# Performance work log

Hardware: AMD Instinct MI355X
Metric: run time of the kernel (lower is better)

## Reference

```python
import jax, jax.numpy as jnp
import numpy as np

N_HEAD = 16
D_IN = 1024
D_OUT = 1024
B, T = 2, 2048
HEAD_DIM = D_OUT // N_HEAD


def setup_inputs() -> dict:
    key = jax.random.key(0)
    ks = jax.random.split(key, 8)
    Q = jax.random.normal(ks[0], (B, T, D_IN), dtype=jnp.float32)
    K = jax.random.normal(ks[1], (B, T, D_IN), dtype=jnp.float32)
    V = jax.random.normal(ks[2], (B, T, D_IN), dtype=jnp.float32)
    mask = jax.random.randint(ks[3], (B, T, T), 0, 2, dtype=jnp.int32)
    s_in = 1.0 / np.sqrt(D_IN)
    s_out = 1.0 / np.sqrt(D_OUT)
    Wq = jax.random.uniform(ks[4], (D_IN, D_OUT), jnp.float32, -s_in, s_in)
    Wk = jax.random.uniform(ks[5], (D_IN, D_OUT), jnp.float32, -s_in, s_in)
    Wv = jax.random.uniform(ks[6], (D_IN, D_OUT), jnp.float32, -s_in, s_in)
    Wo = jax.random.uniform(ks[7], (D_OUT, D_OUT), jnp.float32, -s_out, s_out)
    return {"Q": Q, "K": K, "V": V, "mask": mask,
            "Wq": Wq, "Wk": Wk, "Wv": Wv, "Wo": Wo}


def _split_heads(x):
    b, t, _ = x.shape
    return x.reshape(b, t, N_HEAD, HEAD_DIM).transpose(0, 2, 1, 3)  # [B,H,T,hd]


def reference(Q, K, V, mask, Wq, Wk, Wv, Wo):
    q = _split_heads(Q @ Wq)
    k = _split_heads(K @ Wk)
    v = _split_heads(V @ Wv)
    scale = 1.0 / jnp.sqrt(jnp.float32(HEAD_DIM))  # Q.size(-1) after head split
    scores = jnp.einsum('bhqd,bhkd->bhqk', q, k) * scale  # [B,H,T,T]
    m = mask[:, None, :, :]  # expand over heads
    scores = jnp.where(m == 0, jnp.float32(-1e9), scores)
    attn = jax.nn.softmax(scores, axis=-1)
    z = jnp.einsum('bhqk,bhkd->bhqd', attn, v)  # [B,H,T,hd]
    z = z.transpose(0, 2, 1, 3).reshape(Q.shape[0], T, D_OUT)
    return z @ Wo
```

## Files before the change

### kernel.cpp

```cpp
#include <hip/hip_runtime.h>
#include <math.h>

#define DIN 1024
#define DOUT 1024
#define NHEAD 16
#define HDIM 64
#define BATCH 2
#define TSEQ 2048
#define MROWS (BATCH * TSEQ)

typedef unsigned short u16;
typedef __attribute__((ext_vector_type(8))) short short8;
typedef __attribute__((ext_vector_type(4))) float f32x4;
typedef __attribute__((ext_vector_type(4))) unsigned short us4;

__device__ __forceinline__ void f32_to_bf16pair(float x, u16& hi, u16& lo) {
  unsigned u = __float_as_uint(x);
  unsigned r = (u + 0x7fffu + ((u >> 16) & 1u)) & 0xffff0000u;
  hi = (u16)(r >> 16);
  float rem = x - __uint_as_float(r);
  unsigned u2 = __float_as_uint(rem);
  lo = (u16)((u2 + 0x7fffu + ((u2 >> 16) & 1u)) >> 16);
}

__device__ __forceinline__ void gld_lds16(const void* g, void* l) {
  __builtin_amdgcn_global_load_lds(
      (__attribute__((address_space(1))) void*)g,
      (__attribute__((address_space(3))) void*)l, 16, 0, 0);
}

__global__ __launch_bounds__(256) void splitA(
    const float* __restrict__ S0, const float* __restrict__ S1,
    const float* __restrict__ S2, u16* __restrict__ H0, u16* __restrict__ L0,
    u16* __restrict__ H1, u16* __restrict__ L1, u16* __restrict__ H2,
    u16* __restrict__ L2) {
  const int z = blockIdx.y;
  const float* S = z == 0 ? S0 : z == 1 ? S1 : S2;
  u16* H = z == 0 ? H0 : z == 1 ? H1 : H2;
  u16* L = z == 0 ? L0 : z == 1 ? L1 : L2;
  const size_t i = ((size_t)blockIdx.x * 256 + threadIdx.x) * 4;
  float4 v = *(const float4*)&S[i];
  us4 h4, l4;
  u16 hh, ll;
  f32_to_bf16pair(v.x, hh, ll);
  h4[0] = hh; l4[0] = ll;
  f32_to_bf16pair(v.y, hh, ll);
  h4[1] = hh; l4[1] = ll;
  f32_to_bf16pair(v.z, hh, ll);
  h4[2] = hh; l4[2] = ll;
  f32_to_bf16pair(v.w, hh, ll);
  h4[3] = hh; l4[3] = ll;
  *(us4*)&H[i] = h4;
  *(us4*)&L[i] = l4;
}

__global__ __launch_bounds__(256) void splitWt(
    const float* __restrict__ W0, const float* __restrict__ W1,
    const float* __restrict__ W2, const float* __restrict__ W3,
    u16* __restrict__ H0, u16* __restrict__ L0, u16* __restrict__ H1,
    u16* __restrict__ L1, u16* __restrict__ H2, u16* __restrict__ L2,
    u16* __restrict__ H3, u16* __restrict__ L3) {
  const int z = blockIdx.z;
  const float* W = z == 0 ? W0 : z == 1 ? W1 : z == 2 ? W2 : W3;
  u16* H = z == 0 ? H0 : z == 1 ? H1 : z == 2 ? H2 : H3;
  u16* L = z == 0 ? L0 : z == 1 ? L1 : z == 2 ? L2 : L3;
  __shared__ float ts[64][68];
  const int tid = threadIdx.x;
  const int k0 = blockIdx.y * 64, n0 = blockIdx.x * 64;
  {
    const int kl = tid >> 2, nc = (tid & 3) * 16;
#pragma unroll
    for (int c = 0; c < 4; ++c)
      *(float4*)&ts[kl][nc + c * 4] =
          *(const float4*)&W[(size_t)(k0 + kl) * DOUT + n0 + nc + c * 4];
  }
  __syncthreads();
  const int nl = tid >> 2, kc = (tid & 3) * 16;
#pragma unroll
  for (int g = 0; g < 4; ++g) {
    us4 h4, l4;
#pragma unroll
    for (int j = 0; j < 4; ++j) {
      u16 hh, ll;
      f32_to_bf16pair(ts[kc + g * 4 + j][nl], hh, ll);
      h4[j] = hh;
      l4[j] = ll;
    }
    const size_t idx = (size_t)(n0 + nl) * DIN + k0 + kc + g * 4;
    *(us4*)&H[idx] = h4;
    *(us4*)&L[idx] = l4;
  }
}

struct GemmPtrs {
  const u16* Ah;
  const u16* Al;
  const u16* Bh;
  const u16* Bl;
  u16* Oh;
  u16* Ol;
  int mode;
};
struct GemmArgs {
  GemmPtrs p[3];
};

__global__ __launch_bounds__(256) void gemm_qkv(GemmArgs args) {
  const GemmPtrs P = args.p[blockIdx.z];
  __shared__ alignas(16) u16 Abuf[128 * 64];
  __shared__ alignas(16) u16 Bbuf[128 * 64];
  const int tid = threadIdx.x;
  const int w = tid >> 6, lane = tid & 63;
  const int lr = lane & 15, qd = lane >> 4;
  const int mw = w >> 1, nw = w & 1;
  const int n0 = blockIdx.x * 128, m0 = blockIdx.y * 128;

  const u16* gA[4];
  const u16* gB[4];
  u16* lA[4];
  u16* lB[4];
  {
    const int cl = lane & 7;
#pragma unroll
    for (int is = 0; is < 4; ++is) {
      const int row = is * 32 + w * 8 + (lane >> 3);
      const int cg = cl ^ (row & 7);
      gA[is] = (cg < 4 ? P.Ah : P.Al) + (size_t)(m0 + row) * DIN + (cg & 3) * 8;
      gB[is] = (cg < 4 ? P.Bh : P.Bl) + (size_t)(n0 + row) * DIN + (cg & 3) * 8;
      lA[is] = Abuf + (size_t)(is * 32 + w * 8) * 64;
      lB[is] = Bbuf + (size_t)(is * 32 + w * 8) * 64;
    }
  }

  f32x4 acc[4][4] = {};

  for (int kt = 0; kt < 32; ++kt) {
    __syncthreads();
#pragma unroll
    for (int is = 0; is < 4; ++is) {
      gld_lds16(gA[is], lA[is]);
      gld_lds16(gB[is], lB[is]);
      gA[is] += 32;
      gB[is] += 32;
    }
    __syncthreads();

    short8 af[4][2], bf[4][2];
#pragma unroll
    for (int t = 0; t < 4; ++t) {
      const int ra = mw * 64 + t * 16 + lr;
      af[t][0] = *(const short8*)&Abuf[ra * 64 + ((qd ^ (ra & 7)) << 3)];
      af[t][1] = *(const short8*)&Abuf[ra * 64 + (((qd + 4) ^ (ra & 7)) << 3)];
      const int rb = nw * 64 + t * 16 + lr;
      bf[t][0] = *(const short8*)&Bbuf[rb * 64 + ((qd ^ (rb & 7)) << 3)];
      bf[t][1] = *(const short8*)&Bbuf[rb * 64 + (((qd + 4) ^ (rb & 7)) << 3)];
    }
#pragma unroll
    for (int mt = 0; mt < 4; ++mt)
#pragma unroll
      for (int nt = 0; nt < 4; ++nt) {
        acc[mt][nt] = __builtin_amdgcn_mfma_f32_16x16x32_bf16(
            af[mt][0], bf[nt][0], acc[mt][nt], 0, 0, 0);
        acc[mt][nt] = __builtin_amdgcn_mfma_f32_16x16x32_bf16(
            af[mt][0], bf[nt][1], acc[mt][nt], 0, 0, 0);
        acc[mt][nt] = __builtin_amdgcn_mfma_f32_16x16x32_bf16(
            af[mt][1], bf[nt][0], acc[mt][nt], 0, 0, 0);
      }
  }

#pragma unroll
  for (int mt = 0; mt < 4; ++mt)
#pragma unroll
    for (int nt = 0; nt < 4; ++nt)
#pragma unroll
      for (int r = 0; r < 4; ++r) {
        const float val = acc[mt][nt][r];
        const int gm = m0 + mw * 64 + mt * 16 + qd * 4 + r;
        const int gn = n0 + nw * 64 + nt * 16 + lr;
        u16 hh16, ll16;
        f32_to_bf16pair(val, hh16, ll16);
        const int bb = gm >> 11, t = gm & 2047;
        const int h = gn >> 6, d = gn & 63;
        size_t idx;
        if (P.mode == 0)
          idx = (((size_t)(bb * NHEAD + h) * TSEQ) + t) * HDIM + d;
        else
          idx = (((size_t)(bb * NHEAD + h) * HDIM) + d) * TSEQ + t;
        P.Oh[idx] = hh16;
        P.Ol[idx] = ll16;
      }
}

__global__ __launch_bounds__(256) void gemm_out(
    const u16* __restrict__ Ah, const u16* __restrict__ Al,
    const u16* __restrict__ Bh, const u16* __restrict__ Bl,
    float* __restrict__ C0, float* __restrict__ C1) {
  float* Of = blockIdx.z == 0 ? C0 : C1;
  const int koff = blockIdx.z * 512;
  __shared__ alignas(16) u16 Abuf[128 * 64];
  __shared__ alignas(16) u16 Bbuf[128 * 64];
  const int tid = threadIdx.x;
  const int w = tid >> 6, lane = tid & 63;
  const int lr = lane & 15, qd = lane >> 4;
  const int mw = w >> 1, nw = w & 1;
  const int n0 = blockIdx.x * 128, m0 = blockIdx.y * 128;

  const u16* gA[4];
  const u16* gB[4];
  u16* lA[4];
  u16* lB[4];
  {
    const int cl = lane & 7;
#pragma unroll
    for (int is = 0; is < 4; ++is) {
      const int row = is * 32 + w * 8 + (lane >> 3);
      const int cg = cl ^ (row & 7);
      gA[is] = (cg < 4 ? Ah : Al) + (size_t)(m0 + row) * DIN + (cg & 3) * 8 + koff;
      gB[is] = (cg < 4 ? Bh : Bl) + (size_t)(n0 + row) * DIN + (cg & 3) * 8 + koff;
      lA[is] = Abuf + (size_t)(is * 32 + w * 8) * 64;
      lB[is] = Bbuf + (size_t)(is * 32 + w * 8) * 64;
    }
  }

  f32x4 acc[4][4] = {};

  for (int kt = 0; kt < 16; ++kt) {
    __syncthreads();
#pragma unroll
    for (int is = 0; is < 4; ++is) {
      gld_lds16(gA[is], lA[is]);
      gld_lds16(gB[is], lB[is]);
      gA[is] += 32;
      gB[is] += 32;
    }
    __syncthreads();

    short8 af[4][2], bf[4][2];
#pragma unroll
    for (int t = 0; t < 4; ++t) {
      const int ra = mw * 64 + t * 16 + lr;
      af[t][0] = *(const short8*)&Abuf[ra * 64 + ((qd ^ (ra & 7)) << 3)];
      af[t][1] = *(const short8*)&Abuf[ra * 64 + (((qd + 4) ^ (ra & 7)) << 3)];
      const int rb = nw * 64 + t * 16 + lr;
      bf[t][0] = *(const short8*)&Bbuf[rb * 64 + ((qd ^ (rb & 7)) << 3)];
      bf[t][1] = *(const short8*)&Bbuf[rb * 64 + (((qd + 4) ^ (rb & 7)) << 3)];
    }
#pragma unroll
    for (int mt = 0; mt < 4; ++mt)
#pragma unroll
      for (int nt = 0; nt < 4; ++nt) {
        acc[mt][nt] = __builtin_amdgcn_mfma_f32_16x16x32_bf16(
            af[mt][0], bf[nt][0], acc[mt][nt], 0, 0, 0);
        acc[mt][nt] = __builtin_amdgcn_mfma_f32_16x16x32_bf16(
            af[mt][0], bf[nt][1], acc[mt][nt], 0, 0, 0);
        acc[mt][nt] = __builtin_amdgcn_mfma_f32_16x16x32_bf16(
            af[mt][1], bf[nt][0], acc[mt][nt], 0, 0, 0);
      }
  }

#pragma unroll
  for (int mt = 0; mt < 4; ++mt)
#pragma unroll
    for (int nt = 0; nt < 4; ++nt)
#pragma unroll
      for (int r = 0; r < 4; ++r) {
        const int gm = m0 + mw * 64 + mt * 16 + qd * 4 + r;
        const int gn = n0 + nw * 64 + nt * 16 + lr;
        Of[(size_t)gm * DOUT + gn] = acc[mt][nt][r];
      }
}

__global__ __launch_bounds__(256) void sumC(const float* __restrict__ A,
                                            const float* __restrict__ B,
                                            float* __restrict__ O) {
  const size_t i = ((size_t)blockIdx.x * 256 + threadIdx.x) * 4;
  float4 a = *(const float4*)&A[i];
  float4 b = *(const float4*)&B[i];
  *(float4*)&O[i] = make_float4(a.x + b.x, a.y + b.y, a.z + b.z, a.w + b.w);
}

template <int MODE>
__global__ __launch_bounds__(256) void gemm64(const float* __restrict__ A,
                                              const float* __restrict__ W,
                                              void* __restrict__ Y0,
                                              void* __restrict__ Y1) {
  __shared__ float As[16][68];
  __shared__ float Bs[16][68];
  const int tid = threadIdx.x;
  const int tx = tid & 15, ty = tid >> 4;
  const int r0 = ty * 4, c0 = tx * 4;
  const int gm0 = blockIdx.x * 64;
  const int gn0 = blockIdx.y * 64;
  const int am = tid >> 2;
  const int ak0 = (tid & 3) * 4;
  const int bk = tid >> 4;
  const int bc = (tid & 15) * 4;
  float acc[4][4] = {};
  for (int k0 = 0; k0 < DIN; k0 += 16) {
    __syncthreads();
    alignas(16) float av[4];
    *(float4*)av = *(const float4*)&A[(size_t)(gm0 + am) * DIN + k0 + ak0];
    As[ak0 + 0][am] = av[0];
    As[ak0 + 1][am] = av[1];
    As[ak0 + 2][am] = av[2];
    As[ak0 + 3][am] = av[3];
    *(float4*)&Bs[bk][bc] = *(const float4*)&W[(size_t)(k0 + bk) * DOUT + gn0 + bc];
    __syncthreads();
#pragma unroll
    for (int kk = 0; kk < 16; ++kk) {
      alignas(16) float a[4], b[4];
      *(float4*)a = *(const float4*)&As[kk][r0];
      *(float4*)b = *(const float4*)&Bs[kk][c0];
#pragma unroll
      for (int i = 0; i < 4; ++i)
#pragma unroll
        for (int j = 0; j < 4; ++j) acc[i][j] += a[i] * b[j];
    }
  }
  if constexpr (MODE == 1) {
    float* Y = (float*)Y0;
#pragma unroll
    for (int i = 0; i < 4; ++i) {
      float4 o = make_float4(acc[i][0], acc[i][1], acc[i][2], acc[i][3]);
      *(float4*)&Y[(size_t)(gm0 + r0 + i) * DOUT + gn0 + c0] = o;
    }
  } else if constexpr (MODE == 0) {
    u16* Yh = (u16*)Y0;
    u16* Yl = (u16*)Y1;
    const int bb = gm0 >> 11, tb = gm0 & 2047, h = gn0 >> 6;
#pragma unroll
    for (int i = 0; i < 4; ++i) {
      us4 h4, l4;
#pragma unroll
      for (int j = 0; j < 4; ++j) {
        u16 hh, ll;
        f32_to_bf16pair(acc[i][j], hh, ll);
        h4[j] = hh;
        l4[j] = ll;
      }
      size_t idx = (((size_t)(bb * NHEAD + h) * TSEQ) + tb + r0 + i) * HDIM + c0;
      *(us4*)&Yh[idx] = h4;
      *(us4*)&Yl[idx] = l4;
    }
  } else {
    __shared__ float ts[64][68];
#pragma unroll
    for (int i = 0; i < 4; ++i) {
      float4 o = make_float4(acc[i][0], acc[i][1], acc[i][2], acc[i][3]);
      *(float4*)&ts[r0 + i][c0] = o;
    }
    __syncthreads();
    u16* Yh = (u16*)Y0;
    u16* Yl = (u16*)Y1;
    const int bb = gm0 >> 11, tb = gm0 & 2047, h = gn0 >> 6;
    const int d = tid >> 2;
    const int t0 = (tid & 3) * 16;
#pragma unroll
    for (int g = 0; g < 4; ++g) {
      us4 h4, l4;
#pragma unroll
      for (int j = 0; j < 4; ++j) {
        u16 hh, ll;
        f32_to_bf16pair(ts[t0 + g * 4 + j][d], hh, ll);
        h4[j] = hh;
        l4[j] = ll;
      }
      size_t idx = (((size_t)(bb * NHEAD + h) * HDIM) + d) * TSEQ + tb + t0 + g * 4;
      *(us4*)&Yh[idx] = h4;
      *(us4*)&Yl[idx] = l4;
    }
  }
}

template <int EPI>
__global__ __launch_bounds__(256, 4) void attn64q(
    const u16* __restrict__ qh, const u16* __restrict__ ql,
    const u16* __restrict__ kh, const u16* __restrict__ kl,
    const u16* __restrict__ vh, const u16* __restrict__ vl,
    const int* __restrict__ mask, float* __restrict__ zf,
    u16* __restrict__ zh, u16* __restrict__ zl) {
  __shared__ alignas(16) u16 lds_k[2][64 * 64];
  __shared__ alignas(16) u16 lds_v[2][64 * 64];
  __shared__ alignas(16) u16 lds_p[4][16 * 64];
  const int tid = threadIdx.x;
  const int w = tid >> 6, lane = tid & 63;
  const int lr = lane & 15, qd = lane >> 4;
  const int L = blockIdx.x;
  const int bh = (L & 7) + 8 * ((L >> 3) & 3);
  const int qt0 = (L >> 5) * 64;
  const int bb = bh >> 4, hh = bh & 15;
  const int wq0 = qt0 + w * 16;
  const size_t bh_off = (size_t)bh * TSEQ * HDIM;

  short8 qf[2][2];
#pragma unroll
  for (int ks = 0; ks < 2; ++ks) {
    const size_t off = bh_off + (size_t)(wq0 + lr) * HDIM + ks * 32 + qd * 8;
    qf[ks][0] = *(const short8*)(qh + off);
    qf[ks][1] = *(const short8*)(ql + off);
  }

  f32x4 zacc[4] = {};
  float lsum[4] = {};

  const u16* ssrc = (w == 0 ? kh : w == 1 ? kl : w == 2 ? vh : vl) + bh_off;
  u16* sdst = (w < 2) ? &lds_k[w][0] : &lds_v[w - 2][0];
  const bool isk = (w < 2);
  const int srow = lane >> 3, scl = lane & 7;
  const int* mrow = mask + ((size_t)bb * TSEQ + wq0 + qd * 4) * TSEQ + lr;

  for (int kt0 = 0; kt0 < TSEQ; kt0 += 64) {
    __syncthreads();
#pragma unroll
    for (int is = 0; is < 8; ++is) {
      const int row = is * 8 + srow;
      const int cg = scl ^ (row & 7);
      const u16* src = isk ? ssrc + (size_t)(kt0 + row) * HDIM + cg * 8
                           : ssrc + (size_t)row * TSEQ + kt0 + cg * 8;
      gld_lds16(src, sdst + is * 512);
    }
    __syncthreads();

    int mv[4][4];
#pragma unroll
    for (int r = 0; r < 4; ++r) {
      const int* mr = mrow + (size_t)r * TSEQ + kt0;
#pragma unroll
      for (int nt = 0; nt < 4; ++nt) mv[nt][r] = mr[nt * 16];
    }

    f32x4 sacc[4] = {};
#pragma unroll
    for (int ks = 0; ks < 2; ++ks)
#pragma unroll
      for (int nt = 0; nt < 4; ++nt) {
        const int krow = nt * 16 + lr;
        const int chunk = (((ks * 4 + qd) ^ (krow & 7)) << 3);
        short8 bhf = *(const short8*)&lds_k[0][krow * 64 + chunk];
        short8 blf = *(const short8*)&lds_k[1][krow * 64 + chunk];
        sacc[nt] = __builtin_amdgcn_mfma_f32_16x16x32_bf16(qf[ks][0], bhf,
                                                           sacc[nt], 0, 0, 0);
        sacc[nt] = __builtin_amdgcn_mfma_f32_16x16x32_bf16(qf[ks][0], blf,
                                                           sacc[nt], 0, 0, 0);
        sacc[nt] = __builtin_amdgcn_mfma_f32_16x16x32_bf16(qf[ks][1], bhf,
                                                           sacc[nt], 0, 0, 0);
      }

    u16* pw = &lds_p[w][0];
#pragma unroll
    for (int nt = 0; nt < 4; ++nt)
#pragma unroll
      for (int r = 0; r < 4; ++r) {
        float s = sacc[nt][r];
        s = mv[nt][r] ? s * 0.125f : -1.0e9f;
        float p = __expf(s);
        unsigned u = (__float_as_uint(p) + 0x8000u) & 0xffff0000u;
        lsum[r] += __uint_as_float(u);
        const int prow = qd * 4 + r;
        const int pcol = nt * 16 + lr;
        pw[prow * 64 + ((((pcol >> 3) ^ (prow & 7)) << 3)) + (pcol & 7)] =
            (u16)(u >> 16);
      }

#pragma unroll
    for (int ks = 0; ks < 2; ++ks) {
      const int chunkp = (((ks * 4 + qd) ^ (lr & 7)) << 3);
      short8 pf = *(const short8*)&pw[lr * 64 + chunkp];
#pragma unroll
      for (int nt = 0; nt < 4; ++nt) {
        const int vrow = nt * 16 + lr;
        const int chunk = (((ks * 4 + qd) ^ (vrow & 7)) << 3);
        short8 vhf = *(const short8*)&lds_v[0][vrow * 64 + chunk];
        short8 vlf = *(const short8*)&lds_v[1][vrow * 64 + chunk];
        zacc[nt] = __builtin_amdgcn_mfma_f32_16x16x32_bf16(pf, vhf, zacc[nt],
                                                           0, 0, 0);
        zacc[nt] = __builtin_amdgcn_mfma_f32_16x16x32_bf16(pf, vlf, zacc[nt],
                                                           0, 0, 0);
      }
    }
  }

#pragma unroll
  for (int r = 0; r < 4; ++r) {
    float v = lsum[r];
#pragma unroll
    for (int off = 1; off < 16; off <<= 1) v += __shfl_xor(v, off);
    lsum[r] = 1.0f / v;
  }
#pragma unroll
  for (int r = 0; r < 4; ++r) {
    const int qrow = wq0 + qd * 4 + r;
#pragma unroll
    for (int nt = 0; nt < 4; ++nt) {
      const float val = zacc[nt][r] * lsum[r];
      const size_t idx =
          ((size_t)bb * TSEQ + qrow) * DOUT + hh * HDIM + nt * 16 + lr;
      if (EPI == 0) {
        zf[idx] = val;
      } else {
        u16 hh16, ll16;
        f32_to_bf16pair(val, hh16, ll16);
        zh[idx] = hh16;
        zl[idx] = ll16;
      }
    }
  }
}

extern "C" void kernel_launch(void* const* d_in, const int* in_sizes, int n_in,
                              void* d_out, int out_size, void* d_ws,
                              size_t ws_size, hipStream_t stream) {
  const float* Q = (const float*)d_in[0];
  const float* K = (const float*)d_in[1];
  const float* V = (const float*)d_in[2];
  const int* mask = (const int*)d_in[3];
  const float* Wq = (const float*)d_in[4];
  const float* Wk = (const float*)d_in[5];
  const float* Wv = (const float*)d_in[6];
  const float* Wo = (const float*)d_in[7];
  float* out = (float*)d_out;
  dim3 blk(256);

  if (ws_size >= (size_t)134217728) {
    u16* base = (u16*)d_ws;
    auto U = [&](size_t mib) { return base + mib * 524288; };
    u16 *Qh = U(0), *Ql = U(8), *Kh = U(16), *Kl = U(24), *Vh = U(32),
        *Vl = U(40);
    u16 *Wqh = U(48), *Wql = U(50), *Wkh = U(52), *Wkl = U(54), *Wvh = U(56),
        *Wvl = U(58), *Woh = U(60), *Wol = U(62);
    u16 *qh = U(64), *ql = U(72), *kh = U(80), *kl = U(88), *vth = U(96),
        *vtl = U(104);
    u16 *zh = U(112), *zl = U(120);
    float* C0 = (float*)U(0);
    float* C1 = (float*)U(16);

    splitA<<<dim3(4096, 3), blk, 0, stream>>>(Q, K, V, Qh, Ql, Kh, Kl, Vh, Vl);
    splitWt<<<dim3(16, 16, 4), blk, 0, stream>>>(Wq, Wk, Wv, Wo, Wqh, Wql, Wkh,
                                                 Wkl, Wvh, Wvl, Woh, Wol);
    GemmArgs ga;
    ga.p[0] = {Qh, Ql, Wqh, Wql, qh, ql, 0};
    ga.p[1] = {Kh, Kl, Wkh, Wkl, kh, kl, 0};
    ga.p[2] = {Vh, Vl, Wvh, Wvl, vth, vtl, 2};
    gemm_qkv<<<dim3(8, 32, 3), blk, 0, stream>>>(ga);
    attn64q<1><<<dim3(1024), blk, 0, stream>>>(qh, ql, kh, kl, vth, vtl, mask,
                                               nullptr, zh, zl);
    gemm_out<<<dim3(8, 32, 2), blk, 0, stream>>>(zh, zl, Woh, Wol, C0, C1);
    sumC<<<dim3(4096), blk, 0, stream>>>(C0, C1, out);
  } else {
    const size_t NE = (size_t)MROWS * DOUT;
    u16* qhb = (u16*)d_ws;
    u16* qlb = qhb + NE;
    u16* khb = qlb + NE;
    u16* klb = khb + NE;
    u16* vth = klb + NE;
    u16* vtl = vth + NE;
    float* zb = (float*)(vtl + NE);
    dim3 gg(MROWS / 64, DOUT / 64);
    gemm64<0><<<gg, blk, 0, stream>>>(Q, Wq, qhb, qlb);
    gemm64<0><<<gg, blk, 0, stream>>>(K, Wk, khb, klb);
    gemm64<2><<<gg, blk, 0, stream>>>(V, Wv, vth, vtl);
    attn64q<0><<<dim3(1024), blk, 0, stream>>>(qhb, qlb, khb, klb, vth, vtl,
                                               mask, zb, nullptr, nullptr);
    gemm64<1><<<gg, blk, 0, stream>>>(zb, Wo, (void*)out, nullptr);
  }
}
```

Measured before the change: 409.6 us.

## Fuse fp32 input bf16 split into QKV GEMM and bit-pack attention mask

The QKV GEMM now loads fp32 activations straight into LDS and splits them into bf16 hi/lo pairs in registers, so the separate splitA pass and its writes and re-reads of hi/lo arrays go away. A new mask_pack kernel packs the int32 mask into 64-bit ballot words, so the attention kernel reads 1 bit per mask entry instead of 4 bytes. The small-workspace fallback path is removed. The trade-off is redundant conversion ALU work in every GEMM tile (each A tile is re-split by every N-block) plus one extra launch for mask packing.

```diff
diff --git a/kernel.cpp b/kernel.cpp
--- a/kernel.cpp
+++ b/kernel.cpp
@@ -10,6 +10,7 @@
 #define MROWS (BATCH * TSEQ)
 
 typedef unsigned short u16;
+typedef unsigned long long u64;
 typedef __attribute__((ext_vector_type(8))) short short8;
 typedef __attribute__((ext_vector_type(4))) float f32x4;
 typedef __attribute__((ext_vector_type(4))) unsigned short us4;
@@ -29,29 +30,18 @@
       (__attribute__((address_space(3))) void*)l, 16, 0, 0);
 }
 
-__global__ __launch_bounds__(256) void splitA(
-    const float* __restrict__ S0, const float* __restrict__ S1,
-    const float* __restrict__ S2, u16* __restrict__ H0, u16* __restrict__ L0,
-    u16* __restrict__ H1, u16* __restrict__ L1, u16* __restrict__ H2,
-    u16* __restrict__ L2) {
-  const int z = blockIdx.y;
-  const float* S = z == 0 ? S0 : z == 1 ? S1 : S2;
-  u16* H = z == 0 ? H0 : z == 1 ? H1 : H2;
-  u16* L = z == 0 ? L0 : z == 1 ? L1 : L2;
-  const size_t i = ((size_t)blockIdx.x * 256 + threadIdx.x) * 4;
-  float4 v = *(const float4*)&S[i];
-  us4 h4, l4;
-  u16 hh, ll;
-  f32_to_bf16pair(v.x, hh, ll);
-  h4[0] = hh; l4[0] = ll;
-  f32_to_bf16pair(v.y, hh, ll);
-  h4[1] = hh; l4[1] = ll;
-  f32_to_bf16pair(v.z, hh, ll);
-  h4[2] = hh; l4[2] = ll;
-  f32_to_bf16pair(v.w, hh, ll);
-  h4[3] = hh; l4[3] = ll;
-  *(us4*)&H[i] = h4;
-  *(us4*)&L[i] = l4;
+__global__ __launch_bounds__(256) void mask_pack(const int* __restrict__ mask,
+                                                 u64* __restrict__ bits) {
+  const int gw = blockIdx.x * 4 + (threadIdx.x >> 6);
+  const int lane = threadIdx.x & 63;
+  const int* row = mask + (size_t)gw * TSEQ;
+  u64* orow = bits + (size_t)gw * (TSEQ / 64);
+#pragma unroll 4
+  for (int kt = 0; kt < TSEQ / 64; ++kt) {
+    int m = row[kt * 64 + lane];
+    u64 b = __ballot(m != 0);
+    if (lane == 0) orow[kt] = b;
+  }
 }
 
 __global__ __launch_bounds__(256) void splitWt(
@@ -92,22 +82,21 @@
   }
 }
 
-struct GemmPtrs {
-  const u16* Ah;
-  const u16* Al;
+struct QkvPtrs {
+  const float* Af;
   const u16* Bh;
   const u16* Bl;
   u16* Oh;
   u16* Ol;
   int mode;
 };
-struct GemmArgs {
-  GemmPtrs p[3];
+struct QkvArgs {
+  QkvPtrs p[3];
 };
 
-__global__ __launch_bounds__(256) void gemm_qkv(GemmArgs args) {
-  const GemmPtrs P = args.p[blockIdx.z];
-  __shared__ alignas(16) u16 Abuf[128 * 64];
+__global__ __launch_bounds__(256) void gemm_qkv(QkvArgs args) {
+  const QkvPtrs P = args.p[blockIdx.z];
+  __shared__ alignas(16) float Abuf[128 * 32];
   __shared__ alignas(16) u16 Bbuf[128 * 64];
   const int tid = threadIdx.x;
   const int w = tid >> 6, lane = tid & 63;
@@ -115,9 +104,9 @@
   const int mw = w >> 1, nw = w & 1;
   const int n0 = blockIdx.x * 128, m0 = blockIdx.y * 128;
 
-  const u16* gA[4];
+  const float* gA[4];
   const u16* gB[4];
-  u16* lA[4];
+  float* lA[4];
   u16* lB[4];
   {
     const int cl = lane & 7;
@@ -125,9 +114,9 @@
     for (int is = 0; is < 4; ++is) {
       const int row = is * 32 + w * 8 + (lane >> 3);
       const int cg = cl ^ (row & 7);
-      gA[is] = (cg < 4 ? P.Ah : P.Al) + (size_t)(m0 + row) * DIN + (cg & 3) * 8;
+      gA[is] = P.Af + (size_t)(m0 + row) * DIN + cg * 4;
       gB[is] = (cg < 4 ? P.Bh : P.Bl) + (size_t)(n0 + row) * DIN + (cg & 3) * 8;
-      lA[is] = Abuf + (size_t)(is * 32 + w * 8) * 64;
+      lA[is] = Abuf + (size_t)(is * 32 + w * 8) * 32;
       lB[is] = Bbuf + (size_t)(is * 32 + w * 8) * 64;
     }
   }
@@ -145,26 +134,41 @@
     }
     __syncthreads();
 
-    short8 af[4][2], bf[4][2];
+    short8 afh[4], afl[4];
 #pragma unroll
     for (int t = 0; t < 4; ++t) {
       const int ra = mw * 64 + t * 16 + lr;
-      af[t][0] = *(const short8*)&Abuf[ra * 64 + ((qd ^ (ra & 7)) << 3)];
-      af[t][1] = *(const short8*)&Abuf[ra * 64 + (((qd + 4) ^ (ra & 7)) << 3)];
+      const float* rp = &Abuf[ra * 32];
+      f32x4 a0 = *(const f32x4*)&rp[(((2 * qd) ^ (ra & 7)) * 4)];
+      f32x4 a1 = *(const f32x4*)&rp[(((2 * qd + 1) ^ (ra & 7)) * 4)];
+#pragma unroll
+      for (int j = 0; j < 4; ++j) {
+        u16 hh, ll;
+        f32_to_bf16pair(a0[j], hh, ll);
+        afh[t][j] = (short)hh;
+        afl[t][j] = (short)ll;
+        f32_to_bf16pair(a1[j], hh, ll);
+        afh[t][4 + j] = (short)hh;
+        afl[t][4 + j] = (short)ll;
+      }
+    }
+    short8 bfh[4], bfl[4];
+#pragma unroll
+    for (int t = 0; t < 4; ++t) {
       const int rb = nw * 64 + t * 16 + lr;
-      bf[t][0] = *(const short8*)&Bbuf[rb * 64 + ((qd ^ (rb & 7)) << 3)];
-      bf[t][1] = *(const short8*)&Bbuf[rb * 64 + (((qd + 4) ^ (rb & 7)) << 3)];
+      bfh[t] = *(const short8*)&Bbuf[rb * 64 + ((qd ^ (rb & 7)) << 3)];
+      bfl[t] = *(const short8*)&Bbuf[rb * 64 + (((qd + 4) ^ (rb & 7)) << 3)];
     }
 #pragma unroll
     for (int mt = 0; mt < 4; ++mt)
 #pragma unroll
       for (int nt = 0; nt < 4; ++nt) {
         acc[mt][nt] = __builtin_amdgcn_mfma_f32_16x16x32_bf16(
-            af[mt][0], bf[nt][0], acc[mt][nt], 0, 0, 0);
-        acc[mt][nt] = __builtin_amdgcn_mfma_f32_16x16x32_bf16(
-            af[mt][0], bf[nt][1], acc[mt][nt], 0, 0, 0);
-        acc[mt][nt] = __builtin_amdgcn_mfma_f32_16x16x32_bf16(
-            af[mt][1], bf[nt][0], acc[mt][nt], 0, 0, 0);
+            afh[mt], bfh[nt], acc[mt][nt], 0, 0, 0);
+        acc[mt][nt] = __builtin_amdgcn_mfma_f32_16x16x32_bf16(
+            afh[mt], bfl[nt], acc[mt][nt], 0, 0, 0);
+        acc[mt][nt] = __builtin_amdgcn_mfma_f32_16x16x32_bf16(
+            afl[mt], bfh[nt], acc[mt][nt], 0, 0, 0);
       }
   }
 
@@ -279,106 +283,12 @@
   *(float4*)&O[i] = make_float4(a.x + b.x, a.y + b.y, a.z + b.z, a.w + b.w);
 }
 
-template <int MODE>
-__global__ __launch_bounds__(256) void gemm64(const float* __restrict__ A,
-                                              const float* __restrict__ W,
-                                              void* __restrict__ Y0,
-                                              void* __restrict__ Y1) {
-  __shared__ float As[16][68];
-  __shared__ float Bs[16][68];
-  const int tid = threadIdx.x;
-  const int tx = tid & 15, ty = tid >> 4;
-  const int r0 = ty * 4, c0 = tx * 4;
-  const int gm0 = blockIdx.x * 64;
-  const int gn0 = blockIdx.y * 64;
-  const int am = tid >> 2;
-  const int ak0 = (tid & 3) * 4;
-  const int bk = tid >> 4;
-  const int bc = (tid & 15) * 4;
-  float acc[4][4] = {};
-  for (int k0 = 0; k0 < DIN; k0 += 16) {
-    __syncthreads();
-    alignas(16) float av[4];
-    *(float4*)av = *(const float4*)&A[(size_t)(gm0 + am) * DIN + k0 + ak0];
-    As[ak0 + 0][am] = av[0];
-    As[ak0 + 1][am] = av[1];
-    As[ak0 + 2][am] = av[2];
-    As[ak0 + 3][am] = av[3];
-    *(float4*)&Bs[bk][bc] = *(const float4*)&W[(size_t)(k0 + bk) * DOUT + gn0 + bc];
-    __syncthreads();
-#pragma unroll
-    for (int kk = 0; kk < 16; ++kk) {
-      alignas(16) float a[4], b[4];
-      *(float4*)a = *(const float4*)&As[kk][r0];
-      *(float4*)b = *(const float4*)&Bs[kk][c0];
-#pragma unroll
-      for (int i = 0; i < 4; ++i)
-#pragma unroll
-        for (int j = 0; j < 4; ++j) acc[i][j] += a[i] * b[j];
-    }
-  }
-  if constexpr (MODE == 1) {
-    float* Y = (float*)Y0;
-#pragma unroll
-    for (int i = 0; i < 4; ++i) {
-      float4 o = make_float4(acc[i][0], acc[i][1], acc[i][2], acc[i][3]);
-      *(float4*)&Y[(size_t)(gm0 + r0 + i) * DOUT + gn0 + c0] = o;
-    }
-  } else if constexpr (MODE == 0) {
-    u16* Yh = (u16*)Y0;
-    u16* Yl = (u16*)Y1;
-    const int bb = gm0 >> 11, tb = gm0 & 2047, h = gn0 >> 6;
-#pragma unroll
-    for (int i = 0; i < 4; ++i) {
-      us4 h4, l4;
-#pragma unroll
-      for (int j = 0; j < 4; ++j) {
-        u16 hh, ll;
-        f32_to_bf16pair(acc[i][j], hh, ll);
-        h4[j] = hh;
-        l4[j] = ll;
-      }
-      size_t idx = (((size_t)(bb * NHEAD + h) * TSEQ) + tb + r0 + i) * HDIM + c0;
-      *(us4*)&Yh[idx] = h4;
-      *(us4*)&Yl[idx] = l4;
-    }
-  } else {
-    __shared__ float ts[64][68];
-#pragma unroll
-    for (int i = 0; i < 4; ++i) {
-      float4 o = make_float4(acc[i][0], acc[i][1], acc[i][2], acc[i][3]);
-      *(float4*)&ts[r0 + i][c0] = o;
-    }
-    __syncthreads();
-    u16* Yh = (u16*)Y0;
-    u16* Yl = (u16*)Y1;
-    const int bb = gm0 >> 11, tb = gm0 & 2047, h = gn0 >> 6;
-    const int d = tid >> 2;
-    const int t0 = (tid & 3) * 16;
-#pragma unroll
-    for (int g = 0; g < 4; ++g) {
-      us4 h4, l4;
-#pragma unroll
-      for (int j = 0; j < 4; ++j) {
-        u16 hh, ll;
-        f32_to_bf16pair(ts[t0 + g * 4 + j][d], hh, ll);
-        h4[j] = hh;
-        l4[j] = ll;
-      }
-      size_t idx = (((size_t)(bb * NHEAD + h) * HDIM) + d) * TSEQ + tb + t0 + g * 4;
-      *(us4*)&Yh[idx] = h4;
-      *(us4*)&Yl[idx] = l4;
-    }
-  }
-}
-
-template <int EPI>
 __global__ __launch_bounds__(256, 4) void attn64q(
     const u16* __restrict__ qh, const u16* __restrict__ ql,
     const u16* __restrict__ kh, const u16* __restrict__ kl,
     const u16* __restrict__ vh, const u16* __restrict__ vl,
-    const int* __restrict__ mask, float* __restrict__ zf,
-    u16* __restrict__ zh, u16* __restrict__ zl) {
+    const u64* __restrict__ bits, u16* __restrict__ zh,
+    u16* __restrict__ zl) {
   __shared__ alignas(16) u16 lds_k[2][64 * 64];
   __shared__ alignas(16) u16 lds_v[2][64 * 64];
   __shared__ alignas(16) u16 lds_p[4][16 * 64];
@@ -407,7 +317,7 @@
   u16* sdst = (w < 2) ? &lds_k[w][0] : &lds_v[w - 2][0];
   const bool isk = (w < 2);
   const int srow = lane >> 3, scl = lane & 7;
-  const int* mrow = mask + ((size_t)bb * TSEQ + wq0 + qd * 4) * TSEQ + lr;
+  const u64* brow = bits + ((size_t)bb * TSEQ + wq0 + qd * 4) * (TSEQ / 64);
 
   for (int kt0 = 0; kt0 < TSEQ; kt0 += 64) {
     __syncthreads();
@@ -421,13 +331,9 @@
     }
     __syncthreads();
 
-    int mv[4][4];
-#pragma unroll
-    for (int r = 0; r < 4; ++r) {
-      const int* mr = mrow + (size_t)r * TSEQ + kt0;
-#pragma unroll
-      for (int nt = 0; nt < 4; ++nt) mv[nt][r] = mr[nt * 16];
-    }
+    u64 bm[4];
+#pragma unroll
+    for (int r = 0; r < 4; ++r) bm[r] = brow[r * (TSEQ / 64) + (kt0 >> 6)];
 
     f32x4 sacc[4] = {};
 #pragma unroll
@@ -452,7 +358,8 @@
 #pragma unroll
       for (int r = 0; r < 4; ++r) {
         float s = sacc[nt][r];
-        s = mv[nt][r] ? s * 0.125f : -1.0e9f;
+        const unsigned keep = (unsigned)(bm[r] >> (nt * 16 + lr)) & 1u;
+        s = keep ? s * 0.125f : -1.0e9f;
         float p = __expf(s);
         unsigned u = (__float_as_uint(p) + 0x8000u) & 0xffff0000u;
         lsum[r] += __uint_as_float(u);
@@ -495,14 +402,10 @@
       const float val = zacc[nt][r] * lsum[r];
       const size_t idx =
           ((size_t)bb * TSEQ + qrow) * DOUT + hh * HDIM + nt * 16 + lr;
-      if (EPI == 0) {
-        zf[idx] = val;
-      } else {
-        u16 hh16, ll16;
-        f32_to_bf16pair(val, hh16, ll16);
-        zh[idx] = hh16;
-        zl[idx] = ll16;
-      }
+      u16 hh16, ll16;
+      f32_to_bf16pair(val, hh16, ll16);
+      zh[idx] = hh16;
+      zl[idx] = ll16;
     }
   }
 }
@@ -521,46 +424,27 @@
   float* out = (float*)d_out;
   dim3 blk(256);
 
-  if (ws_size >= (size_t)134217728) {
-    u16* base = (u16*)d_ws;
-    auto U = [&](size_t mib) { return base + mib * 524288; };
-    u16 *Qh = U(0), *Ql = U(8), *Kh = U(16), *Kl = U(24), *Vh = U(32),
-        *Vl = U(40);
-    u16 *Wqh = U(48), *Wql = U(50), *Wkh = U(52), *Wkl = U(54), *Wvh = U(56),
-        *Wvl = U(58), *Woh = U(60), *Wol = U(62);
-    u16 *qh = U(64), *ql = U(72), *kh = U(80), *kl = U(88), *vth = U(96),
-        *vtl = U(104);
-    u16 *zh = U(112), *zl = U(120);
-    float* C0 = (float*)U(0);
-    float* C1 = (float*)U(16);
-
-    splitA<<<dim3(4096, 3), blk, 0, stream>>>(Q, K, V, Qh, Ql, Kh, Kl, Vh, Vl);
-    splitWt<<<dim3(16, 16, 4), blk, 0, stream>>>(Wq, Wk, Wv, Wo, Wqh, Wql, Wkh,
-                                                 Wkl, Wvh, Wvl, Woh, Wol);
-    GemmArgs ga;
-    ga.p[0] = {Qh, Ql, Wqh, Wql, qh, ql, 0};
-    ga.p[1] = {Kh, Kl, Wkh, Wkl, kh, kl, 0};
-    ga.p[2] = {Vh, Vl, Wvh, Wvl, vth, vtl, 2};
-    gemm_qkv<<<dim3(8, 32, 3), blk, 0, stream>>>(ga);
-    attn64q<1><<<dim3(1024), blk, 0, stream>>>(qh, ql, kh, kl, vth, vtl, mask,
-                                               nullptr, zh, zl);
-    gemm_out<<<dim3(8, 32, 2), blk, 0, stream>>>(zh, zl, Woh, Wol, C0, C1);
-    sumC<<<dim3(4096), blk, 0, stream>>>(C0, C1, out);
-  } else {
-    const size_t NE = (size_t)MROWS * DOUT;
-    u16* qhb = (u16*)d_ws;
-    u16* qlb = qhb + NE;
-    u16* khb = qlb + NE;
-    u16* klb = khb + NE;
-    u16* vth = klb + NE;
-    u16* vtl = vth + NE;
-    float* zb = (float*)(vtl + NE);
-    dim3 gg(MROWS / 64, DOUT / 64);
-    gemm64<0><<<gg, blk, 0, stream>>>(Q, Wq, qhb, qlb);
-    gemm64<0><<<gg, blk, 0, stream>>>(K, Wk, khb, klb);
-    gemm64<2><<<gg, blk, 0, stream>>>(V, Wv, vth, vtl);
-    attn64q<0><<<dim3(1024), blk, 0, stream>>>(qhb, qlb, khb, klb, vth, vtl,
-                                               mask, zb, nullptr, nullptr);
-    gemm64<1><<<gg, blk, 0, stream>>>(zb, Wo, (void*)out, nullptr);
-  }
-}
+  u16* base = (u16*)d_ws;
+  auto U = [&](size_t mib) { return base + mib * 524288; };
+  float* C0 = (float*)U(0);
+  float* C1 = (float*)U(16);
+  u64* bits = (u64*)U(32);
+  u16 *Wqh = U(48), *Wql = U(50), *Wkh = U(52), *Wkl = U(54), *Wvh = U(56),
+      *Wvl = U(58), *Woh = U(60), *Wol = U(62);
+  u16 *qh = U(64), *ql = U(72), *kh = U(80), *kl = U(88), *vth = U(96),
+      *vtl = U(104);
+  u16 *zh = U(112), *zl = U(120);
+
+  mask_pack<<<dim3(1024), blk, 0, stream>>>(mask, bits);
+  splitWt<<<dim3(16, 16, 4), blk, 0, stream>>>(Wq, Wk, Wv, Wo, Wqh, Wql, Wkh,
+                                               Wkl, Wvh, Wvl, Woh, Wol);
+  QkvArgs ga;
+  ga.p[0] = {Q, Wqh, Wql, qh, ql, 0};
+  ga.p[1] = {K, Wkh, Wkl, kh, kl, 0};
+  ga.p[2] = {V, Wvh, Wvl, vth, vtl, 2};
+  gemm_qkv<<<dim3(8, 32, 3), blk, 0, stream>>>(ga);
+  attn64q<<<dim3(1024), blk, 0, stream>>>(qh, ql, kh, kl, vth, vtl, bits, zh,
+                                          zl);
+  gemm_out<<<dim3(8, 32, 2), blk, 0, stream>>>(zh, zl, Woh, Wol, C0, C1);
+  sumC<<<dim3(4096), blk, 0, stream>>>(C0, C1, out);
+}
```

Measured after the change: 453.4 us. 1.11x slower.
